# Performance work log

Hardware: AMD Instinct MI355X
Metric: run time of the kernel (lower is better)

## Reference

```python
import jax, jax.numpy as jnp
import numpy as np


def setup_inputs() -> dict:
    key = jax.random.key(0)
    B, H = 8192, 32768
    x = jax.random.normal(key, (B, H), dtype=jnp.float32)
    return {"hidden_preactivation_BH": x, "k": 64}


def reference(hidden_preactivation_BH, k):
    # top-k along last dim, then scatter values back into a zero tensor
    vals_BK, idx_BK = jax.lax.top_k(hidden_preactivation_BH, k)
    B = hidden_preactivation_BH.shape[0]
    rows_B1 = jnp.arange(B)[:, None]
    out_BH = jnp.zeros_like(hidden_preactivation_BH)
    out_BH = out_BH.at[rows_B1, idx_BK].set(vals_BK)
    return out_BH
```

## Files before the change

kernel.cpp:

```cpp
#include <hip/hip_runtime.h>
#include <stdint.h>

#define TPB 512
#define NJ 16
#define HSZ 32768
#define CAP 2048

__device__ __forceinline__ uint32_t f2k(float f) {
    uint32_t u = __float_as_uint(f);
    return u ^ (0x80000000u | (uint32_t)(-(int32_t)(u >> 31)));
}
__device__ __forceinline__ float k2f(uint32_t key) {
    uint32_t u = (key & 0x80000000u) ? (key ^ 0x80000000u) : ~key;
    return __uint_as_float(u);
}

__device__ __forceinline__ void select4096(const uint32_t* hist, uint32_t need,
                                           uint32_t* wtot, uint32_t* sh_bin,
                                           uint32_t* sh_rem, int t) {
    const int lane = t & 63, wid = t >> 6;
    uint32_t b[8], pt = 0;
#pragma unroll
    for (int jj = 0; jj < 8; ++jj) { b[jj] = hist[t * 8 + jj]; pt += b[jj]; }
    uint32_t pre = pt;
#pragma unroll
    for (int off = 1; off < 64; off <<= 1) {
        uint32_t n = (uint32_t)__shfl_down((int)pre, off, 64);
        if (lane + off < 64) pre += n;
    }
    if (lane == 0) wtot[wid] = pre;
    __syncthreads();
    uint32_t wsuf = 0;
    for (int w = wid + 1; w < TPB / 64; ++w) wsuf += wtot[w];
    const uint32_t Sincl = pre + wsuf;
    const uint32_t Sexcl = Sincl - pt;
    if (Sexcl < need && Sincl >= need) {
        uint32_t run = Sexcl;
#pragma unroll
        for (int jj = 7; jj >= 0; --jj) {
            if (run + b[jj] >= need) { *sh_bin = (uint32_t)(t * 8 + jj); *sh_rem = need - run; break; }
            run += b[jj];
        }
    }
    __syncthreads();
}

__device__ __forceinline__ void select256(const uint32_t* hist, uint32_t need,
                                          uint32_t* wtot, uint32_t* sh_bin,
                                          uint32_t* sh_rem, uint32_t* sh_eqcnt, int t) {
    const int lane = t & 63, wid = t >> 6;
    uint32_t pt = (t < 256) ? hist[t] : 0u;
    uint32_t pre = pt;
#pragma unroll
    for (int off = 1; off < 64; off <<= 1) {
        uint32_t n = (uint32_t)__shfl_down((int)pre, off, 64);
        if (lane + off < 64) pre += n;
    }
    if (lane == 0) wtot[wid] = pre;
    __syncthreads();
    uint32_t wsuf = 0;
    for (int w = wid + 1; w < TPB / 64; ++w) wsuf += wtot[w];
    const uint32_t Sincl = pre + wsuf;
    const uint32_t Sexcl = Sincl - pt;
    if (t < 256 && Sexcl < need && Sincl >= need) {
        *sh_bin = (uint32_t)t; *sh_rem = need - Sexcl; *sh_eqcnt = pt;
    }
    __syncthreads();
}

__global__ __launch_bounds__(TPB, 4) void topk_scatter_kernel(
    const float* __restrict__ x,
    const int* __restrict__ kp,
    float* __restrict__ out)
{
    __shared__ uint32_t hist[4096];
    __shared__ uint32_t wtot[TPB / 64];
    __shared__ uint32_t cand_key[CAP];
    __shared__ uint32_t cand_col[CAP];
    __shared__ uint32_t sh_bin, sh_rem, sh_eqcnt, sh_ncand;
    __shared__ uint32_t chunk_base;

    const int t = threadIdx.x;
    const size_t row = blockIdx.x;
    const float* xr = x + row * (size_t)HSZ;
    float* outr = out + row * (size_t)HSZ;
    const uint32_t k = (uint32_t)kp[0];

    if (k == 0u || k >= (uint32_t)HSZ) {
#pragma unroll 4
        for (int j = 0; j < NJ; ++j) {
            float4 o;
            if (k == 0u) { o.x = o.y = o.z = o.w = 0.0f; }
            else o = reinterpret_cast<const float4*>(xr)[j * TPB + t];
            reinterpret_cast<float4*>(outr)[j * TPB + t] = o;
        }
        return;
    }

    for (int i = t; i < 4096; i += TPB) hist[i] = 0u;
    if (t == 0) sh_ncand = 0u;
    __syncthreads();
#pragma unroll 4
    for (int j = 0; j < NJ; ++j) {
        float4 v = reinterpret_cast<const float4*>(xr)[j * TPB + t];
        atomicAdd(&hist[f2k(v.x) >> 20], 1u);
        atomicAdd(&hist[f2k(v.y) >> 20], 1u);
        atomicAdd(&hist[f2k(v.z) >> 20], 1u);
        atomicAdd(&hist[f2k(v.w) >> 20], 1u);
    }
    __syncthreads();
    select4096(hist, k, wtot, &sh_bin, &sh_rem, t);
    const uint32_t B1 = sh_bin;
    const uint32_t need2 = sh_rem;

#pragma unroll 4
    for (int j = 0; j < NJ; ++j) {
        float4 v = reinterpret_cast<const float4*>(xr)[j * TPB + t];
        float vals[4] = { v.x, v.y, v.z, v.w };
        float ov[4];
#pragma unroll
        for (int c = 0; c < 4; ++c) {
            uint32_t key = f2k(vals[c]);
            uint32_t b = key >> 20;
            ov[c] = (b > B1) ? vals[c] : 0.0f;
            if (b == B1) {
                uint32_t pos = atomicAdd(&sh_ncand, 1u);
                if (pos < CAP) {
                    cand_key[pos] = key;
                    cand_col[pos] = (uint32_t)((j * TPB + t) * 4 + c);
                }
            }
        }
        float4 o; o.x = ov[0]; o.y = ov[1]; o.z = ov[2]; o.w = ov[3];
        reinterpret_cast<float4*>(outr)[j * TPB + t] = o;
    }
    __syncthreads();
    const uint32_t C = sh_ncand;

    if (C <= CAP) {
        for (int i = t; i < 4096; i += TPB) hist[i] = 0u;
        __syncthreads();
        for (uint32_t i = t; i < C; i += TPB)
            atomicAdd(&hist[(cand_key[i] >> 8) & 0xFFFu], 1u);
        __syncthreads();
        select4096(hist, need2, wtot, &sh_bin, &sh_rem, t);
        const uint32_t B2 = sh_bin;
        const uint32_t need3 = sh_rem;

        if (t < 256) hist[t] = 0u;
        __syncthreads();
        const uint32_t pref = (B1 << 12) | B2;
        for (uint32_t i = t; i < C; i += TPB)
            if ((cand_key[i] >> 8) == pref) atomicAdd(&hist[cand_key[i] & 0xFFu], 1u);
        __syncthreads();
        select256(hist, need3, wtot, &sh_bin, &sh_rem, &sh_eqcnt, t);
        const uint32_t K = (pref << 8) | sh_bin;
        const uint32_t eqneed = sh_rem;
        const uint32_t eqcnt = sh_eqcnt;

        for (uint32_t i = t; i < C; i += TPB) {
            uint32_t key = cand_key[i];
            if (key > K) {
                outr[cand_col[i]] = k2f(key);
            } else if (key == K) {
                if (eqcnt == eqneed) {
                    outr[cand_col[i]] = k2f(key);
                } else {
                    uint32_t rank = 0, col = cand_col[i];
                    for (uint32_t m = 0; m < C; ++m)
                        if (cand_key[m] == K && cand_col[m] < col) ++rank;
                    if (rank < eqneed) outr[cand_col[i]] = k2f(key);
                }
            }
        }
    } else {
        for (int i = t; i < 4096; i += TPB) hist[i] = 0u;
        __syncthreads();
        for (int j = 0; j < NJ; ++j) {
            float4 v = reinterpret_cast<const float4*>(xr)[j * TPB + t];
            float vals[4] = { v.x, v.y, v.z, v.w };
#pragma unroll
            for (int c = 0; c < 4; ++c) {
                uint32_t key = f2k(vals[c]);
                if ((key >> 20) == B1) atomicAdd(&hist[(key >> 8) & 0xFFFu], 1u);
            }
        }
        __syncthreads();
        select4096(hist, need2, wtot, &sh_bin, &sh_rem, t);
        const uint32_t B2 = sh_bin;
        const uint32_t need3 = sh_rem;

        if (t < 256) hist[t] = 0u;
        __syncthreads();
        const uint32_t pref = (B1 << 12) | B2;
        for (int j = 0; j < NJ; ++j) {
            float4 v = reinterpret_cast<const float4*>(xr)[j * TPB + t];
            float vals[4] = { v.x, v.y, v.z, v.w };
#pragma unroll
            for (int c = 0; c < 4; ++c) {
                uint32_t key = f2k(vals[c]);
                if ((key >> 8) == pref) atomicAdd(&hist[key & 0xFFu], 1u);
            }
        }
        __syncthreads();
        select256(hist, need3, wtot, &sh_bin, &sh_rem, &sh_eqcnt, t);
        const uint32_t K = (pref << 8) | sh_bin;
        const uint32_t eqneed = sh_rem;
        const uint32_t eqcnt = sh_eqcnt;

        if (eqcnt == eqneed) {
            for (int j = 0; j < NJ; ++j) {
                float4 v = reinterpret_cast<const float4*>(xr)[j * TPB + t];
                float vals[4] = { v.x, v.y, v.z, v.w };
                float ov[4];
#pragma unroll
                for (int c = 0; c < 4; ++c)
                    ov[c] = (f2k(vals[c]) >= K) ? vals[c] : 0.0f;
                float4 o; o.x = ov[0]; o.y = ov[1]; o.z = ov[2]; o.w = ov[3];
                reinterpret_cast<float4*>(outr)[j * TPB + t] = o;
            }
        } else {
            if (t == 0) chunk_base = 0u;
            __syncthreads();
            const int lane = t & 63;
            const int wid = t >> 6;
            for (int j = 0; j < NJ; ++j) {
                float4 v = reinterpret_cast<const float4*>(xr)[j * TPB + t];
                float vals[4] = { v.x, v.y, v.z, v.w };
                uint32_t keys[4];
                uint32_t e = 0;
#pragma unroll
                for (int c = 0; c < 4; ++c) { keys[c] = f2k(vals[c]); e += (keys[c] == K) ? 1u : 0u; }
                uint32_t pre = e;
                for (int off = 1; off < 64; off <<= 1) {
                    uint32_t n = (uint32_t)__shfl_up((int)pre, off, 64);
                    if (lane >= off) pre += n;
                }
                if (lane == 63) wtot[wid] = pre;
                __syncthreads();
                uint32_t before = chunk_base + (pre - e);
                for (int w = 0; w < wid; ++w) before += wtot[w];
                float ov[4];
#pragma unroll
                for (int c = 0; c < 4; ++c) {
                    bool take = keys[c] > K;
                    if (keys[c] == K) { take = (before < eqneed); ++before; }
                    ov[c] = take ? vals[c] : 0.0f;
                }
                float4 o; o.x = ov[0]; o.y = ov[1]; o.z = ov[2]; o.w = ov[3];
                reinterpret_cast<float4*>(outr)[j * TPB + t] = o;
                __syncthreads();
                if (t == 0) {
                    uint32_t s2 = chunk_base;
#pragma unroll
                    for (int w = 0; w < TPB / 64; ++w) s2 += wtot[w];
                    chunk_base = s2;
                }
                __syncthreads();
            }
        }
    }
}

extern "C" void kernel_launch(void* const* d_in, const int* in_sizes, int n_in,
                              void* d_out, int out_size, void* d_ws, size_t ws_size,
                              hipStream_t stream) {
    const float* x = (const float*)d_in[0];
    const int* kp = (const int*)d_in[1];
    float* out = (float*)d_out;
    const int total = in_sizes[0];
    const int rows = total / HSZ;
    topk_scatter_kernel<<<rows, TPB, 0, stream>>>(x, kp, out);
}
```

Measured before the change: 533.4 us.

## Cache row in registers and double block size to read input once

Raises the block to 1024 threads so each thread holds only 8 float4 values, then loads the row into registers once and reuses them for the histogram, candidate and output passes instead of re-reading global memory. This removes the second full read of each 128 KB row, which matters for this memory-bound kernel. In exchange, register pressure rises (32 floats per thread kept live), occupancy is limited by 1024-thread blocks, and select4096 is adjusted to 4 bins per thread.

```diff
diff --git a/kernel.cpp b/kernel.cpp
--- a/kernel.cpp
+++ b/kernel.cpp
@@ -1,9 +1,10 @@
 #include <hip/hip_runtime.h>
 #include <stdint.h>
 
-#define TPB 512
-#define NJ 16
+#define TPB 1024
+#define NJ 8
 #define HSZ 32768
+#define NW (TPB / 64)
 #define CAP 2048
 
 __device__ __forceinline__ uint32_t f2k(float f) {
@@ -19,9 +20,9 @@
                                            uint32_t* wtot, uint32_t* sh_bin,
                                            uint32_t* sh_rem, int t) {
     const int lane = t & 63, wid = t >> 6;
-    uint32_t b[8], pt = 0;
-#pragma unroll
-    for (int jj = 0; jj < 8; ++jj) { b[jj] = hist[t * 8 + jj]; pt += b[jj]; }
+    uint32_t b[4], pt = 0;
+#pragma unroll
+    for (int jj = 0; jj < 4; ++jj) { b[jj] = hist[t * 4 + jj]; pt += b[jj]; }
     uint32_t pre = pt;
 #pragma unroll
     for (int off = 1; off < 64; off <<= 1) {
@@ -31,14 +32,14 @@
     if (lane == 0) wtot[wid] = pre;
     __syncthreads();
     uint32_t wsuf = 0;
-    for (int w = wid + 1; w < TPB / 64; ++w) wsuf += wtot[w];
+    for (int w = wid + 1; w < NW; ++w) wsuf += wtot[w];
     const uint32_t Sincl = pre + wsuf;
     const uint32_t Sexcl = Sincl - pt;
     if (Sexcl < need && Sincl >= need) {
         uint32_t run = Sexcl;
 #pragma unroll
-        for (int jj = 7; jj >= 0; --jj) {
-            if (run + b[jj] >= need) { *sh_bin = (uint32_t)(t * 8 + jj); *sh_rem = need - run; break; }
+        for (int jj = 3; jj >= 0; --jj) {
+            if (run + b[jj] >= need) { *sh_bin = (uint32_t)(t * 4 + jj); *sh_rem = need - run; break; }
             run += b[jj];
         }
     }
@@ -59,7 +60,7 @@
     if (lane == 0) wtot[wid] = pre;
     __syncthreads();
     uint32_t wsuf = 0;
-    for (int w = wid + 1; w < TPB / 64; ++w) wsuf += wtot[w];
+    for (int w = wid + 1; w < NW; ++w) wsuf += wtot[w];
     const uint32_t Sincl = pre + wsuf;
     const uint32_t Sexcl = Sincl - pt;
     if (t < 256 && Sexcl < need && Sincl >= need) {
@@ -74,7 +75,7 @@
     float* __restrict__ out)
 {
     __shared__ uint32_t hist[4096];
-    __shared__ uint32_t wtot[TPB / 64];
+    __shared__ uint32_t wtot[NW];
     __shared__ uint32_t cand_key[CAP];
     __shared__ uint32_t cand_col[CAP];
     __shared__ uint32_t sh_bin, sh_rem, sh_eqcnt, sh_ncand;
@@ -82,41 +83,44 @@
 
     const int t = threadIdx.x;
     const size_t row = blockIdx.x;
-    const float* xr = x + row * (size_t)HSZ;
+    const float4* xr4 = reinterpret_cast<const float4*>(x + row * (size_t)HSZ);
     float* outr = out + row * (size_t)HSZ;
+    float4* outr4 = reinterpret_cast<float4*>(outr);
     const uint32_t k = (uint32_t)kp[0];
 
     if (k == 0u || k >= (uint32_t)HSZ) {
-#pragma unroll 4
+#pragma unroll
         for (int j = 0; j < NJ; ++j) {
             float4 o;
             if (k == 0u) { o.x = o.y = o.z = o.w = 0.0f; }
-            else o = reinterpret_cast<const float4*>(xr)[j * TPB + t];
-            reinterpret_cast<float4*>(outr)[j * TPB + t] = o;
+            else o = xr4[j * TPB + t];
+            outr4[j * TPB + t] = o;
         }
         return;
     }
+
+    float4 vv[NJ];
+#pragma unroll
+    for (int j = 0; j < NJ; ++j) vv[j] = xr4[j * TPB + t];
 
     for (int i = t; i < 4096; i += TPB) hist[i] = 0u;
     if (t == 0) sh_ncand = 0u;
     __syncthreads();
-#pragma unroll 4
+#pragma unroll
     for (int j = 0; j < NJ; ++j) {
-        float4 v = reinterpret_cast<const float4*>(xr)[j * TPB + t];
-        atomicAdd(&hist[f2k(v.x) >> 20], 1u);
-        atomicAdd(&hist[f2k(v.y) >> 20], 1u);
-        atomicAdd(&hist[f2k(v.z) >> 20], 1u);
-        atomicAdd(&hist[f2k(v.w) >> 20], 1u);
+        atomicAdd(&hist[f2k(vv[j].x) >> 20], 1u);
+        atomicAdd(&hist[f2k(vv[j].y) >> 20], 1u);
+        atomicAdd(&hist[f2k(vv[j].z) >> 20], 1u);
+        atomicAdd(&hist[f2k(vv[j].w) >> 20], 1u);
     }
     __syncthreads();
     select4096(hist, k, wtot, &sh_bin, &sh_rem, t);
     const uint32_t B1 = sh_bin;
     const uint32_t need2 = sh_rem;
 
-#pragma unroll 4
+#pragma unroll
     for (int j = 0; j < NJ; ++j) {
-        float4 v = reinterpret_cast<const float4*>(xr)[j * TPB + t];
-        float vals[4] = { v.x, v.y, v.z, v.w };
+        float vals[4] = { vv[j].x, vv[j].y, vv[j].z, vv[j].w };
         float ov[4];
 #pragma unroll
         for (int c = 0; c < 4; ++c) {
@@ -132,7 +136,7 @@
             }
         }
         float4 o; o.x = ov[0]; o.y = ov[1]; o.z = ov[2]; o.w = ov[3];
-        reinterpret_cast<float4*>(outr)[j * TPB + t] = o;
+        outr4[j * TPB + t] = o;
     }
     __syncthreads();
     const uint32_t C = sh_ncand;
@@ -176,9 +180,9 @@
     } else {
         for (int i = t; i < 4096; i += TPB) hist[i] = 0u;
         __syncthreads();
+#pragma unroll
         for (int j = 0; j < NJ; ++j) {
-            float4 v = reinterpret_cast<const float4*>(xr)[j * TPB + t];
-            float vals[4] = { v.x, v.y, v.z, v.w };
+            float vals[4] = { vv[j].x, vv[j].y, vv[j].z, vv[j].w };
 #pragma unroll
             for (int c = 0; c < 4; ++c) {
                 uint32_t key = f2k(vals[c]);
@@ -193,9 +197,9 @@
         if (t < 256) hist[t] = 0u;
         __syncthreads();
         const uint32_t pref = (B1 << 12) | B2;
+#pragma unroll
         for (int j = 0; j < NJ; ++j) {
-            float4 v = reinterpret_cast<const float4*>(xr)[j * TPB + t];
-            float vals[4] = { v.x, v.y, v.z, v.w };
+            float vals[4] = { vv[j].x, vv[j].y, vv[j].z, vv[j].w };
 #pragma unroll
             for (int c = 0; c < 4; ++c) {
                 uint32_t key = f2k(vals[c]);
@@ -209,15 +213,15 @@
         const uint32_t eqcnt = sh_eqcnt;
 
         if (eqcnt == eqneed) {
+#pragma unroll
             for (int j = 0; j < NJ; ++j) {
-                float4 v = reinterpret_cast<const float4*>(xr)[j * TPB + t];
-                float vals[4] = { v.x, v.y, v.z, v.w };
+                float vals[4] = { vv[j].x, vv[j].y, vv[j].z, vv[j].w };
                 float ov[4];
 #pragma unroll
                 for (int c = 0; c < 4; ++c)
                     ov[c] = (f2k(vals[c]) >= K) ? vals[c] : 0.0f;
                 float4 o; o.x = ov[0]; o.y = ov[1]; o.z = ov[2]; o.w = ov[3];
-                reinterpret_cast<float4*>(outr)[j * TPB + t] = o;
+                outr4[j * TPB + t] = o;
             }
         } else {
             if (t == 0) chunk_base = 0u;
@@ -225,8 +229,7 @@
             const int lane = t & 63;
             const int wid = t >> 6;
             for (int j = 0; j < NJ; ++j) {
-                float4 v = reinterpret_cast<const float4*>(xr)[j * TPB + t];
-                float vals[4] = { v.x, v.y, v.z, v.w };
+                float vals[4] = { vv[j].x, vv[j].y, vv[j].z, vv[j].w };
                 uint32_t keys[4];
                 uint32_t e = 0;
 #pragma unroll
@@ -248,12 +251,12 @@
                     ov[c] = take ? vals[c] : 0.0f;
                 }
                 float4 o; o.x = ov[0]; o.y = ov[1]; o.z = ov[2]; o.w = ov[3];
-                reinterpret_cast<float4*>(outr)[j * TPB + t] = o;
+                outr4[j * TPB + t] = o;
                 __syncthreads();
                 if (t == 0) {
                     uint32_t s2 = chunk_base;
 #pragma unroll
-                    for (int w = 0; w < TPB / 64; ++w) s2 += wtot[w];
+                    for (int w = 0; w < NW; ++w) s2 += wtot[w];
                     chunk_base = s2;
                 }
                 __syncthreads();
```

After: 465.6 us. 1.15x faster.
